# Performance work log

Hardware: AMD Instinct MI355X
Metric: run time of the kernel (lower is better)

## Reference

```python
import jax, jax.numpy as jnp
import numpy as np

ALPHA = 0.2  # LeakyReLU negative slope


def setup_inputs() -> dict:
    key = jax.random.key(0)
    ks = jax.random.split(key, 6)
    B, N, F_in, F_out, H = 16, 1024, 256, 256, 8
    h = jax.random.normal(ks[0], (B, N, F_in), dtype=jnp.float32)
    # Per-head Linear W: weight [F_out, F_in] + bias [F_out], stacked over heads
    W = jax.random.normal(ks[1], (H, F_out, F_in), dtype=jnp.float32) * (1.414 / np.sqrt(F_in))
    bW = jax.random.normal(ks[2], (H, F_out), dtype=jnp.float32) * 0.01
    # Per-head Linear A: weight [1, 2*F_out] split into a1 (acts on Whi) and a2 (acts on Whj), bias bA [1]
    a1 = jax.random.normal(ks[3], (H, F_out), dtype=jnp.float32) * (1.414 / np.sqrt(2 * F_out))
    a2 = jax.random.normal(ks[4], (H, F_out), dtype=jnp.float32) * (1.414 / np.sqrt(2 * F_out))
    bA = jax.random.normal(ks[5], (H,), dtype=jnp.float32) * 0.01
    return {"h": h, "W": W, "bW": bW, "a1": a1, "a2": a2, "bA": bA}


def reference(h, W, bW, a1, a2, bA):
    # h: [B,N,F_in], W: [H,F_out,F_in]
    B, N, _ = h.shape
    H, F_out, _ = W.shape
    Wh = jnp.einsum('bnf,hof->bhno', h, W) + bW[None, :, None, :]  # [B,H,N,F_out]
    # Additive score e_ij = a1.Wh_i + a2.Wh_j + bA  (decomposed; avoids N x N x 2F concat)
    ei = jnp.einsum('bhno,ho->bhn', Wh, a1)  # contribution of row node i
    ej = jnp.einsum('bhno,ho->bhn', Wh, a2)  # contribution of col node j
    e = ei[:, :, :, None] + ej[:, :, None, :] + bA[None, :, None, None]  # [B,H,N,N]
    e = jnp.where(e > 0, e, ALPHA * e)  # LeakyReLU
    att = jax.nn.softmax(e, axis=-1)  # softmax over neighbors j (dropout = identity in eval)
    aWh = jnp.einsum('bhij,bhjo->bhio', att, Wh)  # [B,H,N,F_out]
    out = jax.nn.relu(aWh)  # last=False branch
    out = out.transpose(0, 2, 1, 3).reshape(B, N, H * F_out)  # concat heads on feature dim
    return jax.nn.sigmoid(out)
```

## Files before the change

kernel.cpp:

```cpp
#include <hip/hip_runtime.h>


#define L2E 1.442695041f

typedef _Float16 half8 __attribute__((ext_vector_type(8)));
typedef __fp16 fp16x2 __attribute__((ext_vector_type(2)));
typedef float floatx4 __attribute__((ext_vector_type(4)));

#if __has_builtin(__builtin_amdgcn_exp2f)
#define EXP2F(x) __builtin_amdgcn_exp2f(x)
#else
#define EXP2F(x) exp2f(x)
#endif

static __device__ inline unsigned int pack2(float a, float b) {
    fp16x2 h = __builtin_amdgcn_cvt_pkrtz(a, b);
    return __builtin_bit_cast(unsigned int, h);
}

static __device__ inline int swz(int row, int c) {
    return (row << 6) + ((((c) ^ (row >> 1)) & 3) << 4);
}
static __device__ inline int swz128(int row, int c) {
    return (row << 7) + ((((c) ^ row) & 7) << 4);
}

__global__ __launch_bounds__(512, 2) void wh_kernel(
    const float* __restrict__ hin, const float* __restrict__ W,
    const float* __restrict__ bW, _Float16* __restrict__ WhT,
    const float* __restrict__ a1, const float* __restrict__ a2,
    float* __restrict__ ei, float* __restrict__ ej)
{
    const int bnt  = blockIdx.x;
    const int head = blockIdx.y;
    const int t    = threadIdx.x;
    const int wave = t >> 6, lane = t & 63;
    const int l15 = lane & 15, quad = lane >> 4;

    __shared__ char smem[24576];
    _Float16* As = (_Float16*)smem;
    _Float16* Bs = (_Float16*)(smem + 16384);
    float* bWs   = (float*)smem;
    float* a1s   = (float*)(smem + 1024);
    float* a2s   = (float*)(smem + 2048);
    float* part1 = (float*)(smem + 3072);
    float* part2 = (float*)(smem + 5120);

    const int bn0 = bnt * 128;
    floatx4 acc[4][4];
#pragma unroll
    for (int a = 0; a < 4; a++)
#pragma unroll
        for (int b = 0; b < 4; b++) acc[a][b] = (floatx4)0.0f;

    const int wm = (wave & 3) * 4;
    const int wn = (wave >> 2) * 4;

    const int ar = t >> 1, ah = t & 1;
    const int br = t >> 2, bc = t & 3;
    const float* Wrow = W + (size_t)(head * 256 + ar) * 256 + ah * 16;
    const float* hrow = hin + (size_t)(bn0 + br) * 256 + bc * 8;

    float4 pa0, pa1, pa2, pa3, pb0, pb1;
    {
        const float4* p4 = (const float4*)Wrow;
        pa0 = p4[0]; pa1 = p4[1]; pa2 = p4[2]; pa3 = p4[3];
        const float4* q4 = (const float4*)hrow;
        pb0 = q4[0]; pb1 = q4[1];
    }

    for (int f0 = 0; f0 < 256; f0 += 32) {
        __syncthreads();
        *(uint4*)((char*)As + swz(ar, 2 * ah)) =
            make_uint4(pack2(pa0.x, pa0.y), pack2(pa0.z, pa0.w),
                       pack2(pa1.x, pa1.y), pack2(pa1.z, pa1.w));
        *(uint4*)((char*)As + swz(ar, 2 * ah + 1)) =
            make_uint4(pack2(pa2.x, pa2.y), pack2(pa2.z, pa2.w),
                       pack2(pa3.x, pa3.y), pack2(pa3.z, pa3.w));
        *(uint4*)((char*)Bs + swz(br, bc)) =
            make_uint4(pack2(pb0.x, pb0.y), pack2(pb0.z, pb0.w),
                       pack2(pb1.x, pb1.y), pack2(pb1.z, pb1.w));
        if (f0 < 224) {
            const float4* p4 = (const float4*)(Wrow + f0 + 32);
            pa0 = p4[0]; pa1 = p4[1]; pa2 = p4[2]; pa3 = p4[3];
            const float4* q4 = (const float4*)(hrow + f0 + 32);
            pb0 = q4[0]; pb1 = q4[1];
        }
        __syncthreads();
        half8 af[4], bf[4];
#pragma unroll
        for (int a = 0; a < 4; a++)
            af[a] = *(const half8*)((char*)As + swz((wm + a) * 16 + l15, quad));
#pragma unroll
        for (int b = 0; b < 4; b++)
            bf[b] = *(const half8*)((char*)Bs + swz((wn + b) * 16 + l15, quad));
#pragma unroll
        for (int a = 0; a < 4; a++)
#pragma unroll
            for (int b = 0; b < 4; b++)
                acc[a][b] = __builtin_amdgcn_mfma_f32_16x16x32_f16(af[a], bf[b], acc[a][b], 0, 0, 0);
    }

    __syncthreads();
    if (t < 256) {
        bWs[t] = bW[head * 256 + t];
        a1s[t] = a1[head * 256 + t];
        a2s[t] = a2[head * 256 + t];
    }
    __syncthreads();

    const int bidx = bn0 >> 10;
    const int nbase = bn0 & 1023;
    const int g = wave >> 2;
    const int wmw = wave & 3;
#pragma unroll
    for (int b = 0; b < 4; b++) {
        const int bnl = (wn + b) * 16 + l15;
        const int n = nbase + bnl;
        float p1 = 0.f, p2 = 0.f;
#pragma unroll
        for (int a = 0; a < 4; a++) {
#pragma unroll
            for (int r = 0; r < 4; r++) {
                int o = (wm + a) * 16 + quad * 4 + r;
                float v = acc[a][b][r] + bWs[o];
                WhT[(((size_t)(bidx * 8 + head) * 256 + o) << 10) + n] = (_Float16)v;
                p1 = fmaf(v, a1s[o], p1);
                p2 = fmaf(v, a2s[o], p2);
            }
        }
        p1 += __shfl_xor(p1, 16, 64); p1 += __shfl_xor(p1, 32, 64);
        p2 += __shfl_xor(p2, 16, 64); p2 += __shfl_xor(p2, 32, 64);
        if (lane < 16) {
            part1[g * 256 + wmw * 64 + b * 16 + lane] = p1;
            part2[g * 256 + wmw * 64 + b * 16 + lane] = p2;
        }
    }
    __syncthreads();
    if (t < 128) {
        const int gg = t >> 6, r = t & 63;
        float s1 = 0.f, s2 = 0.f;
#pragma unroll
        for (int w = 0; w < 4; w++) {
            s1 += part1[gg * 256 + w * 64 + r];
            s2 += part2[gg * 256 + w * 64 + r];
        }
        const size_t idx = (size_t)(bidx * 8 + head) * 1024 + nbase + t;
        ei[idx] = s1;
        ej[idx] = s2;
    }
}

__global__ __launch_bounds__(512, 2) void pv_kernel(
    const _Float16* __restrict__ WhT, const float* __restrict__ ei,
    const float* __restrict__ ej, const float* __restrict__ bA,
    float* __restrict__ out)
{
    const int bh = blockIdx.x;
    const int it = blockIdx.y;
    const int b = bh >> 3, head = bh & 7;
    const int t = threadIdx.x;
    const int wave = t >> 6, lane = t & 63;
    const int l15 = lane & 15, quad = lane >> 4;

    __shared__ char smem[53824];
    _Float16* Ap = (_Float16*)smem;
    _Float16* Bp = (_Float16*)(smem + 16384);
    float* ejs  = (float*)(smem + 49152);
    float* lns  = (float*)(smem + 53248);
    float* wred = (float*)(smem + 53760);

    const float* ejrow = ej + bh * 1024;
    float v0 = ejrow[t] * L2E, v1 = ejrow[t + 512] * L2E;
    ejs[t] = v0; ejs[t + 512] = v1;
    float mx = fmaxf(v0, v1);
#pragma unroll
    for (int m = 32; m; m >>= 1) mx = fmaxf(mx, __shfl_xor(mx, m, 64));
    if (lane == 0) wred[wave] = mx;
    __syncthreads();
    float ejmax = wred[0];
#pragma unroll
    for (int w = 1; w < 8; w++) ejmax = fmaxf(ejmax, wred[w]);

    const int i0 = it * 128;
    const int prow = t >> 2, pjb = (t & 3) * 16;
    const float cip = (ei[bh * 1024 + i0 + prow] + bA[head]) * L2E;
    const float tmv = cip + ejmax;
    const float nm = -fmaxf(tmv, 0.2f * tmv);

    const int wr_ = t >> 1, hh = t & 1;
    const _Float16* wrow = WhT + ((size_t)bh << 18) + ((size_t)wr_ << 10) + hh * 32;

    floatx4 acc[4][4], accl[4];
#pragma unroll
    for (int a = 0; a < 4; a++) {
        accl[a] = (floatx4)0.0f;
#pragma unroll
        for (int c = 0; c < 4; c++) acc[a][c] = (floatx4)0.0f;
    }
    const int wm = (wave >> 2) * 4;
    const int wn = (wave & 3) * 4;
    const bool doL = ((wave & 3) == 0);
    const half8 ones = {1, 1, 1, 1, 1, 1, 1, 1};

    uint4 w0, w1, w2, w3;
    { const uint4* s = (const uint4*)wrow; w0 = s[0]; w1 = s[1]; w2 = s[2]; w3 = s[3]; }

    for (int j0 = 0; j0 < 1024; j0 += 64) {
        __syncthreads();
        {
            const float* ejp = ejs + j0 + pjb;
            float p[16];
#pragma unroll
            for (int u = 0; u < 16; u++) {
                float e = cip + ejp[u];
                float lr = fmaxf(e, 0.2f * e);
                p[u] = EXP2F(lr + nm);
            }
            const int c0 = (t & 3) * 2;
            *(uint4*)((char*)Ap + swz128(prow, c0)) =
                make_uint4(pack2(p[0], p[1]), pack2(p[2], p[3]),
                           pack2(p[4], p[5]), pack2(p[6], p[7]));
            *(uint4*)((char*)Ap + swz128(prow, c0 + 1)) =
                make_uint4(pack2(p[8], p[9]), pack2(p[10], p[11]),
                           pack2(p[12], p[13]), pack2(p[14], p[15]));
        }
        {
            const int c0 = 4 * hh;
            *(uint4*)((char*)Bp + swz128(wr_, c0))     = w0;
            *(uint4*)((char*)Bp + swz128(wr_, c0 + 1)) = w1;
            *(uint4*)((char*)Bp + swz128(wr_, c0 + 2)) = w2;
            *(uint4*)((char*)Bp + swz128(wr_, c0 + 3)) = w3;
        }
        if (j0 < 960) {
            const uint4* s = (const uint4*)(wrow + j0 + 64);
            w0 = s[0]; w1 = s[1]; w2 = s[2]; w3 = s[3];
        }
        __syncthreads();
#pragma unroll
        for (int kk = 0; kk < 2; kk++) {
            half8 af[4], bf[4];
#pragma unroll
            for (int a = 0; a < 4; a++)
                af[a] = *(const half8*)((char*)Ap + swz128((wm + a) * 16 + l15, kk * 4 + quad));
#pragma unroll
            for (int c = 0; c < 4; c++)
                bf[c] = *(const half8*)((char*)Bp + swz128((wn + c) * 16 + l15, kk * 4 + quad));
            if (doL) {
#pragma unroll
                for (int a = 0; a < 4; a++)
                    accl[a] = __builtin_amdgcn_mfma_f32_16x16x32_f16(af[a], ones, accl[a], 0, 0, 0);
            }
#pragma unroll
            for (int a = 0; a < 4; a++)
#pragma unroll
                for (int c = 0; c < 4; c++)
                    acc[a][c] = __builtin_amdgcn_mfma_f32_16x16x32_f16(af[a], bf[c], acc[a][c], 0, 0, 0);
        }
    }

    __syncthreads();
    if (doL && l15 == 0) {
#pragma unroll
        for (int a = 0; a < 4; a++)
#pragma unroll
            for (int r = 0; r < 4; r++)
                lns[(wm + a) * 16 + quad * 4 + r] = accl[a][r];
    }
    __syncthreads();

    float rinv[4][4];
#pragma unroll
    for (int a = 0; a < 4; a++)
#pragma unroll
        for (int r = 0; r < 4; r++)
            rinv[a][r] = 1.0f / lns[(wm + a) * 16 + quad * 4 + r];

#pragma unroll
    for (int a = 0; a < 4; a++) {
#pragma unroll
        for (int c = 0; c < 4; c++) {
            int o = (wn + c) * 16 + l15;
#pragma unroll
            for (int r = 0; r < 4; r++) {
                int i = i0 + (wm + a) * 16 + quad * 4 + r;
                float v = acc[a][c][r] * rinv[a][r];
                float rl = fmaxf(v, 0.0f);
                float y = 1.0f / (1.0f + EXP2F(-rl * L2E));
                out[((size_t)(b * 1024 + i) << 11) + head * 256 + o] = y;
            }
        }
    }
}

extern "C" void kernel_launch(void* const* d_in, const int* in_sizes, int n_in,
                              void* d_out, int out_size, void* d_ws, size_t ws_size,
                              hipStream_t stream)
{
    const float* h  = (const float*)d_in[0];
    const float* W  = (const float*)d_in[1];
    const float* bW = (const float*)d_in[2];
    const float* a1 = (const float*)d_in[3];
    const float* a2 = (const float*)d_in[4];
    const float* bA = (const float*)d_in[5];
    float* out = (float*)d_out;

    char* ws = (char*)d_ws;
    _Float16* WhT = (_Float16*)ws;
    float* ei = (float*)(ws + 67108864);
    float* ej = (float*)(ws + 67108864 + 524288);

    hipLaunchKernelGGL(wh_kernel, dim3(128, 8), dim3(512), 0, stream,
                       h, W, bW, WhT, a1, a2, ei, ej);
    hipLaunchKernelGGL(pv_kernel, dim3(128, 8), dim3(512), 0, stream,
                       WhT, ei, ej, bA, out);
}
```

Before: 322.0 us.

## Split output-feature dimension across blocks with 256-thread tiles in both kernels

After: 295.4 us. -8.3%, faster.

```diff
diff --git a/kernel.cpp b/kernel.cpp
--- a/kernel.cpp
+++ b/kernel.cpp
@@ -25,27 +25,30 @@
     return (row << 7) + ((((c) ^ row) & 7) << 4);
 }
 
-__global__ __launch_bounds__(512, 2) void wh_kernel(
+__global__ __launch_bounds__(256, 3) void wh_kernel(
     const float* __restrict__ hin, const float* __restrict__ W,
     const float* __restrict__ bW, _Float16* __restrict__ WhT,
     const float* __restrict__ a1, const float* __restrict__ a2,
-    float* __restrict__ ei, float* __restrict__ ej)
+    float* __restrict__ eiP, float* __restrict__ ejP)
 {
     const int bnt  = blockIdx.x;
-    const int head = blockIdx.y;
+    const int ot   = blockIdx.y;
+    const int head = blockIdx.z;
     const int t    = threadIdx.x;
     const int wave = t >> 6, lane = t & 63;
     const int l15 = lane & 15, quad = lane >> 4;
-
-    __shared__ char smem[24576];
+    const int wmh = wave & 1, wnh = wave >> 1;
+
+    __shared__ char smem[16384];
     _Float16* As = (_Float16*)smem;
-    _Float16* Bs = (_Float16*)(smem + 16384);
+    _Float16* Bs = (_Float16*)(smem + 8192);
     float* bWs   = (float*)smem;
-    float* a1s   = (float*)(smem + 1024);
-    float* a2s   = (float*)(smem + 2048);
-    float* part1 = (float*)(smem + 3072);
-    float* part2 = (float*)(smem + 5120);
-
+    float* a1s   = (float*)(smem + 512);
+    float* a2s   = (float*)(smem + 1024);
+    float* part1 = (float*)(smem + 1536);
+    float* part2 = (float*)(smem + 2560);
+
+    const int o0 = ot * 128;
     const int bn0 = bnt * 128;
     floatx4 acc[4][4];
 #pragma unroll
@@ -53,20 +56,16 @@
 #pragma unroll
         for (int b = 0; b < 4; b++) acc[a][b] = (floatx4)0.0f;
 
-    const int wm = (wave & 3) * 4;
-    const int wn = (wave >> 2) * 4;
-
     const int ar = t >> 1, ah = t & 1;
-    const int br = t >> 2, bc = t & 3;
-    const float* Wrow = W + (size_t)(head * 256 + ar) * 256 + ah * 16;
-    const float* hrow = hin + (size_t)(bn0 + br) * 256 + bc * 8;
-
-    float4 pa0, pa1, pa2, pa3, pb0, pb1;
+    const float* Wrow = W + (size_t)(head * 256 + o0 + ar) * 256 + ah * 16;
+    const float* hrow = hin + (size_t)(bn0 + ar) * 256 + ah * 16;
+
+    float4 pa0, pa1, pa2, pa3, pb0, pb1, pb2, pb3;
     {
         const float4* p4 = (const float4*)Wrow;
         pa0 = p4[0]; pa1 = p4[1]; pa2 = p4[2]; pa3 = p4[3];
         const float4* q4 = (const float4*)hrow;
-        pb0 = q4[0]; pb1 = q4[1];
+        pb0 = q4[0]; pb1 = q4[1]; pb2 = q4[2]; pb3 = q4[3];
     }
 
     for (int f0 = 0; f0 < 256; f0 += 32) {
@@ -77,23 +76,26 @@
         *(uint4*)((char*)As + swz(ar, 2 * ah + 1)) =
             make_uint4(pack2(pa2.x, pa2.y), pack2(pa2.z, pa2.w),
                        pack2(pa3.x, pa3.y), pack2(pa3.z, pa3.w));
-        *(uint4*)((char*)Bs + swz(br, bc)) =
+        *(uint4*)((char*)Bs + swz(ar, 2 * ah)) =
             make_uint4(pack2(pb0.x, pb0.y), pack2(pb0.z, pb0.w),
                        pack2(pb1.x, pb1.y), pack2(pb1.z, pb1.w));
+        *(uint4*)((char*)Bs + swz(ar, 2 * ah + 1)) =
+            make_uint4(pack2(pb2.x, pb2.y), pack2(pb2.z, pb2.w),
+                       pack2(pb3.x, pb3.y), pack2(pb3.z, pb3.w));
         if (f0 < 224) {
             const float4* p4 = (const float4*)(Wrow + f0 + 32);
             pa0 = p4[0]; pa1 = p4[1]; pa2 = p4[2]; pa3 = p4[3];
             const float4* q4 = (const float4*)(hrow + f0 + 32);
-            pb0 = q4[0]; pb1 = q4[1];
+            pb0 = q4[0]; pb1 = q4[1]; pb2 = q4[2]; pb3 = q4[3];
         }
         __syncthreads();
         half8 af[4], bf[4];
 #pragma unroll
         for (int a = 0; a < 4; a++)
-            af[a] = *(const half8*)((char*)As + swz((wm + a) * 16 + l15, quad));
+            af[a] = *(const half8*)((char*)As + swz(wmh * 64 + a * 16 + l15, quad));
 #pragma unroll
         for (int b = 0; b < 4; b++)
-            bf[b] = *(const half8*)((char*)Bs + swz((wn + b) * 16 + l15, quad));
+            bf[b] = *(const half8*)((char*)Bs + swz(wnh * 64 + b * 16 + l15, quad));
 #pragma unroll
         for (int a = 0; a < 4; a++)
 #pragma unroll
@@ -102,94 +104,94 @@
     }
 
     __syncthreads();
-    if (t < 256) {
-        bWs[t] = bW[head * 256 + t];
-        a1s[t] = a1[head * 256 + t];
-        a2s[t] = a2[head * 256 + t];
+    if (t < 128) {
+        bWs[t] = bW[head * 256 + o0 + t];
+        a1s[t] = a1[head * 256 + o0 + t];
+        a2s[t] = a2[head * 256 + o0 + t];
     }
     __syncthreads();
 
     const int bidx = bn0 >> 10;
     const int nbase = bn0 & 1023;
-    const int g = wave >> 2;
-    const int wmw = wave & 3;
 #pragma unroll
     for (int b = 0; b < 4; b++) {
-        const int bnl = (wn + b) * 16 + l15;
+        const int bnl = wnh * 64 + b * 16 + l15;
         const int n = nbase + bnl;
         float p1 = 0.f, p2 = 0.f;
 #pragma unroll
         for (int a = 0; a < 4; a++) {
 #pragma unroll
             for (int r = 0; r < 4; r++) {
-                int o = (wm + a) * 16 + quad * 4 + r;
-                float v = acc[a][b][r] + bWs[o];
-                WhT[(((size_t)(bidx * 8 + head) * 256 + o) << 10) + n] = (_Float16)v;
-                p1 = fmaf(v, a1s[o], p1);
-                p2 = fmaf(v, a2s[o], p2);
+                int ol = wmh * 64 + a * 16 + quad * 4 + r;
+                float v = acc[a][b][r] + bWs[ol];
+                WhT[(((size_t)(bidx * 8 + head) * 256 + o0 + ol) << 10) + n] = (_Float16)v;
+                p1 = fmaf(v, a1s[ol], p1);
+                p2 = fmaf(v, a2s[ol], p2);
             }
         }
         p1 += __shfl_xor(p1, 16, 64); p1 += __shfl_xor(p1, 32, 64);
         p2 += __shfl_xor(p2, 16, 64); p2 += __shfl_xor(p2, 32, 64);
         if (lane < 16) {
-            part1[g * 256 + wmw * 64 + b * 16 + lane] = p1;
-            part2[g * 256 + wmw * 64 + b * 16 + lane] = p2;
+            part1[wmh * 128 + bnl] = p1;
+            part2[wmh * 128 + bnl] = p2;
         }
     }
     __syncthreads();
     if (t < 128) {
-        const int gg = t >> 6, r = t & 63;
-        float s1 = 0.f, s2 = 0.f;
-#pragma unroll
-        for (int w = 0; w < 4; w++) {
-            s1 += part1[gg * 256 + w * 64 + r];
-            s2 += part2[gg * 256 + w * 64 + r];
-        }
+        float s1 = part1[t] + part1[128 + t];
+        float s2 = part2[t] + part2[128 + t];
         const size_t idx = (size_t)(bidx * 8 + head) * 1024 + nbase + t;
-        ei[idx] = s1;
-        ej[idx] = s2;
-    }
-}
-
-__global__ __launch_bounds__(512, 2) void pv_kernel(
-    const _Float16* __restrict__ WhT, const float* __restrict__ ei,
-    const float* __restrict__ ej, const float* __restrict__ bA,
+        eiP[(size_t)ot * 131072 + idx] = s1;
+        ejP[(size_t)ot * 131072 + idx] = s2;
+    }
+}
+
+__global__ __launch_bounds__(256, 3) void pv_kernel(
+    const _Float16* __restrict__ WhT, const float* __restrict__ eiP,
+    const float* __restrict__ ejP, const float* __restrict__ bA,
     float* __restrict__ out)
 {
     const int bh = blockIdx.x;
     const int it = blockIdx.y;
+    const int ot = blockIdx.z;
     const int b = bh >> 3, head = bh & 7;
     const int t = threadIdx.x;
     const int wave = t >> 6, lane = t & 63;
     const int l15 = lane & 15, quad = lane >> 4;
-
-    __shared__ char smem[53824];
+    const int wmh = wave & 1, wnh = wave >> 1;
+
+    __shared__ char smem[37440];
     _Float16* Ap = (_Float16*)smem;
     _Float16* Bp = (_Float16*)(smem + 16384);
-    float* ejs  = (float*)(smem + 49152);
-    float* lns  = (float*)(smem + 53248);
-    float* wred = (float*)(smem + 53760);
-
-    const float* ejrow = ej + bh * 1024;
-    float v0 = ejrow[t] * L2E, v1 = ejrow[t + 512] * L2E;
-    ejs[t] = v0; ejs[t + 512] = v1;
-    float mx = fmaxf(v0, v1);
+    float* ejs  = (float*)(smem + 32768);
+    float* lns  = (float*)(smem + 36864);
+    float* wred = (float*)(smem + 37376);
+
+    const float* ej0 = ejP + bh * 1024;
+    const float* ej1 = ejP + 131072 + bh * 1024;
+    float mx = -1e30f;
+#pragma unroll
+    for (int k = 0; k < 4; k++) {
+        int idx = t + k * 256;
+        float v = (ej0[idx] + ej1[idx]) * L2E;
+        ejs[idx] = v;
+        mx = fmaxf(mx, v);
+    }
 #pragma unroll
     for (int m = 32; m; m >>= 1) mx = fmaxf(mx, __shfl_xor(mx, m, 64));
     if (lane == 0) wred[wave] = mx;
     __syncthreads();
-    float ejmax = wred[0];
-#pragma unroll
-    for (int w = 1; w < 8; w++) ejmax = fmaxf(ejmax, wred[w]);
-
-    const int i0 = it * 128;
-    const int prow = t >> 2, pjb = (t & 3) * 16;
-    const float cip = (ei[bh * 1024 + i0 + prow] + bA[head]) * L2E;
+    float ejmax = fmaxf(fmaxf(wred[0], wred[1]), fmaxf(wred[2], wred[3]));
+
+    const int i0 = it * 128, o0 = ot * 128;
+    const int prow = t >> 1, pjh = t & 1;
+    const float cip = (eiP[bh * 1024 + i0 + prow] +
+                       eiP[131072 + bh * 1024 + i0 + prow] + bA[head]) * L2E;
     const float tmv = cip + ejmax;
     const float nm = -fmaxf(tmv, 0.2f * tmv);
 
     const int wr_ = t >> 1, hh = t & 1;
-    const _Float16* wrow = WhT + ((size_t)bh << 18) + ((size_t)wr_ << 10) + hh * 32;
+    const _Float16* wrow = WhT + ((size_t)bh << 18) + ((size_t)(o0 + wr_) << 10) + hh * 32;
 
     floatx4 acc[4][4], accl[4];
 #pragma unroll
@@ -198,9 +200,7 @@
 #pragma unroll
         for (int c = 0; c < 4; c++) acc[a][c] = (floatx4)0.0f;
     }
-    const int wm = (wave >> 2) * 4;
-    const int wn = (wave & 3) * 4;
-    const bool doL = ((wave & 3) == 0);
+    const bool doL = (wnh == 0);
     const half8 ones = {1, 1, 1, 1, 1, 1, 1, 1};
 
     uint4 w0, w1, w2, w3;
@@ -209,21 +209,23 @@
     for (int j0 = 0; j0 < 1024; j0 += 64) {
         __syncthreads();
         {
-            const float* ejp = ejs + j0 + pjb;
-            float p[16];
-#pragma unroll
-            for (int u = 0; u < 16; u++) {
-                float e = cip + ejp[u];
-                float lr = fmaxf(e, 0.2f * e);
-                p[u] = EXP2F(lr + nm);
+            const float4* ejp4 = (const float4*)(ejs + j0 + pjh * 32);
+#pragma unroll
+            for (int q = 0; q < 4; q++) {
+                float4 e4a = ejp4[2 * q], e4b = ejp4[2 * q + 1];
+                float p[8];
+                const float ev[8] = {e4a.x, e4a.y, e4a.z, e4a.w,
+                                     e4b.x, e4b.y, e4b.z, e4b.w};
+#pragma unroll
+                for (int u = 0; u < 8; u++) {
+                    float e = cip + ev[u];
+                    float lr = fmaxf(e, 0.2f * e);
+                    p[u] = EXP2F(lr + nm);
+                }
+                *(uint4*)((char*)Ap + swz128(prow, pjh * 4 + q)) =
+                    make_uint4(pack2(p[0], p[1]), pack2(p[2], p[3]),
+                               pack2(p[4], p[5]), pack2(p[6], p[7]));
             }
-            const int c0 = (t & 3) * 2;
-            *(uint4*)((char*)Ap + swz128(prow, c0)) =
-                make_uint4(pack2(p[0], p[1]), pack2(p[2], p[3]),
-                           pack2(p[4], p[5]), pack2(p[6], p[7]));
-            *(uint4*)((char*)Ap + swz128(prow, c0 + 1)) =
-                make_uint4(pack2(p[8], p[9]), pack2(p[10], p[11]),
-                           pack2(p[12], p[13]), pack2(p[14], p[15]));
         }
         {
             const int c0 = 4 * hh;
@@ -242,10 +244,10 @@
             half8 af[4], bf[4];
 #pragma unroll
             for (int a = 0; a < 4; a++)
-                af[a] = *(const half8*)((char*)Ap + swz128((wm + a) * 16 + l15, kk * 4 + quad));
+                af[a] = *(const half8*)((char*)Ap + swz128(wmh * 64 + a * 16 + l15, kk * 4 + quad));
 #pragma unroll
             for (int c = 0; c < 4; c++)
-                bf[c] = *(const half8*)((char*)Bp + swz128((wn + c) * 16 + l15, kk * 4 + quad));
+                bf[c] = *(const half8*)((char*)Bp + swz128(wnh * 64 + c * 16 + l15, kk * 4 + quad));
             if (doL) {
 #pragma unroll
                 for (int a = 0; a < 4; a++)
@@ -265,7 +267,7 @@
         for (int a = 0; a < 4; a++)
 #pragma unroll
             for (int r = 0; r < 4; r++)
-                lns[(wm + a) * 16 + quad * 4 + r] = accl[a][r];
+                lns[wmh * 64 + a * 16 + quad * 4 + r] = accl[a][r];
     }
     __syncthreads();
 
@@ -274,16 +276,16 @@
     for (int a = 0; a < 4; a++)
 #pragma unroll
         for (int r = 0; r < 4; r++)
-            rinv[a][r] = 1.0f / lns[(wm + a) * 16 + quad * 4 + r];
+            rinv[a][r] = 1.0f / lns[wmh * 64 + a * 16 + quad * 4 + r];
 
 #pragma unroll
     for (int a = 0; a < 4; a++) {
 #pragma unroll
         for (int c = 0; c < 4; c++) {
-            int o = (wn + c) * 16 + l15;
+            int o = o0 + wnh * 64 + c * 16 + l15;
 #pragma unroll
             for (int r = 0; r < 4; r++) {
-                int i = i0 + (wm + a) * 16 + quad * 4 + r;
+                int i = i0 + wmh * 64 + a * 16 + quad * 4 + r;
                 float v = acc[a][c][r] * rinv[a][r];
                 float rl = fmaxf(v, 0.0f);
                 float y = 1.0f / (1.0f + EXP2F(-rl * L2E));
@@ -307,11 +309,11 @@
 
     char* ws = (char*)d_ws;
     _Float16* WhT = (_Float16*)ws;
-    float* ei = (float*)(ws + 67108864);
-    float* ej = (float*)(ws + 67108864 + 524288);
-
-    hipLaunchKernelGGL(wh_kernel, dim3(128, 8), dim3(512), 0, stream,
-                       h, W, bW, WhT, a1, a2, ei, ej);
-    hipLaunchKernelGGL(pv_kernel, dim3(128, 8), dim3(512), 0, stream,
-                       WhT, ei, ej, bA, out);
-}
+    float* eiP = (float*)(ws + 67108864);
+    float* ejP = (float*)(ws + 67108864 + 1048576);
+
+    hipLaunchKernelGGL(wh_kernel, dim3(128, 2, 8), dim3(256), 0, stream,
+                       h, W, bW, WhT, a1, a2, eiP, ejP);
+    hipLaunchKernelGGL(pv_kernel, dim3(128, 8, 2), dim3(256), 0, stream,
+                       WhT, eiP, ejP, bA, out);
+}
```
